# Kernel optimization log

Measured on AMD Instinct MI355X. Metric: run time of the kernel, lower is better.

Reference implementation:

```python
import jax, jax.numpy as jnp
import numpy as np

BS, R, W, N, H = 256, 4, 128, 2048, 256
TAU, ALPHA, EPS = 1.0, 0.7, 1e-8


def _l2norm(x, axis):
    return x / (jnp.linalg.norm(x, axis=axis, keepdims=True) + EPS)


def _gumbel(u):
    # standard Gumbel(0,1) from uniform samples
    return -jnp.log(-jnp.log(u + 1e-10) + 1e-10)


def setup_inputs() -> dict:
    key = jax.random.key(0)
    ks = jax.random.split(key, 10)
    return {
        "k_r": jax.random.normal(ks[0], (BS, R * W), jnp.float32),
        "m_t": jax.random.normal(ks[1], (BS, W), jnp.float32),
        "hx": jax.random.normal(ks[2], (1, BS, H), jnp.float32),
        "memory": jax.random.uniform(ks[3], (BS, W, N), jnp.float32),
        "usage": jax.random.uniform(ks[4], (BS, N), jnp.float32),
        "read_weights": jax.random.uniform(ks[5], (BS, R, N), jnp.float32),
        "Wg": jax.random.normal(ks[6], (H, 1), jnp.float32) / np.float32(np.sqrt(H)),
        "bg": jnp.zeros((1,), jnp.float32),
        "noise_write": jax.random.uniform(ks[7], (BS, 1, N), jnp.float32),
        "noise_read": jax.random.uniform(ks[8], (BS, R, N), jnp.float32),
        "m_idx": jax.random.randint(ks[9], (BS, N), 0, N).astype(jnp.int64),
        "seq_idx": N,
    }


def reference(k_r, m_t, hx, memory, usage, read_weights, Wg, bg,
              noise_write, noise_read, m_idx, seq_idx):
    # --- key / candidate preprocessing ---
    read_keys = jnp.tanh(k_r.reshape(BS, R, W))   # bs r W
    write_m = jnp.tanh(m_t.reshape(BS, 1, W))     # bs 1 W

    # --- usage bookkeeping (read weights detached as in torch) ---
    u_t = ALPHA * usage + (1.0 - ALPHA) * jax.lax.stop_gradient(read_weights).sum(axis=1)  # bs N

    # --- write (memory-full branch: content-addressed erase/update) ---
    # reversed cosine similarity between candidate and each slot
    dist = jnp.einsum('biw,bwn->bin', _l2norm(write_m, 2), _l2norm(memory, 1))  # bs 1 N
    gamma = jax.nn.sigmoid(hx[-1] @ Wg + bg)                                    # bs 1
    soft_wt = -dist + (gamma * u_t)[:, None, :]                                 # bs 1 N
    write_wt = jax.nn.softmax((1.0 - soft_wt + _gumbel(noise_write)) / TAU, axis=2)  # bs 1 N

    m_erased = jnp.einsum('bin,bwn->biw', write_wt, memory)                     # bs 1 W
    # M * (E - e^T w) + m^T w  with e = ones -> M*(1 - w) + m^T w
    mem_new = memory * (1.0 - write_wt) + jnp.einsum('biw,bin->bwn', write_m, write_wt)
    usage_new = u_t * (1.0 - jax.lax.stop_gradient(write_wt[:, 0, :]))          # bs N

    # --- read (gumbel-softmax content addressing on updated memory) ---
    dist_r = jnp.einsum('brw,bwn->brn', _l2norm(read_keys, 2), _l2norm(mem_new, 1))  # bs r N
    read_wt = jax.nn.softmax((dist_r + _gumbel(noise_read)) / TAU, axis=2)           # bs r N
    m_read = jnp.einsum('brn,bwn->brw', read_wt, mem_new)                            # bs r W

    return (m_read, mem_new, usage_new, read_wt, m_erased)
```

## Files before the change

### kernel.cpp

```cpp
#include <hip/hip_runtime.h>

#define BS   256
#define RR   4
#define WW   128
#define NN   2048
#define HH   256
#define NT   512
#define WH   64
#define NWAVE (NT / 64)
#define RPW  (WH / NWAVE)

typedef float nfloat4 __attribute__((ext_vector_type(4)));

__device__ __forceinline__ float wave_sum(float v) {
#pragma unroll
  for (int m = 32; m >= 1; m >>= 1) v += __shfl_xor(v, m, 64);
  return v;
}
__device__ __forceinline__ float wave_max(float v) {
#pragma unroll
  for (int m = 32; m >= 1; m >>= 1) v = fmaxf(v, __shfl_xor(v, m, 64));
  return v;
}
__device__ __forceinline__ float block_sum(float v, float* s_red) {
  const int tid = threadIdx.x;
  v = wave_sum(v);
  __syncthreads();
  if ((tid & 63) == 0) s_red[tid >> 6] = v;
  __syncthreads();
  float s = s_red[0];
#pragma unroll
  for (int i = 1; i < NWAVE; ++i) s += s_red[i];
  return s;
}
__device__ __forceinline__ float block_max(float v, float* s_red) {
  const int tid = threadIdx.x;
  v = wave_max(v);
  __syncthreads();
  if ((tid & 63) == 0) s_red[tid >> 6] = v;
  __syncthreads();
  float s = s_red[0];
#pragma unroll
  for (int i = 1; i < NWAVE; ++i) s = fmaxf(s, s_red[i]);
  return s;
}
__device__ __forceinline__ void block_max4(float v[RR], float* s_red4) {
  const int tid = threadIdx.x, lane = tid & 63, wid = tid >> 6;
#pragma unroll
  for (int m = 32; m >= 1; m >>= 1) {
#pragma unroll
    for (int r = 0; r < RR; ++r) v[r] = fmaxf(v[r], __shfl_xor(v[r], m, 64));
  }
  __syncthreads();
  if (lane == 0) {
#pragma unroll
    for (int r = 0; r < RR; ++r) s_red4[wid * RR + r] = v[r];
  }
  __syncthreads();
#pragma unroll
  for (int r = 0; r < RR; ++r) {
    float s = s_red4[r];
#pragma unroll
    for (int i = 1; i < NWAVE; ++i) s = fmaxf(s, s_red4[i * RR + r]);
    v[r] = s;
  }
}
__device__ __forceinline__ void block_sum4(float v[RR], float* s_red4) {
  const int tid = threadIdx.x, lane = tid & 63, wid = tid >> 6;
#pragma unroll
  for (int m = 32; m >= 1; m >>= 1) {
#pragma unroll
    for (int r = 0; r < RR; ++r) v[r] += __shfl_xor(v[r], m, 64);
  }
  __syncthreads();
  if (lane == 0) {
#pragma unroll
    for (int r = 0; r < RR; ++r) s_red4[wid * RR + r] = v[r];
  }
  __syncthreads();
#pragma unroll
  for (int r = 0; r < RR; ++r) {
    float s = s_red4[r];
#pragma unroll
    for (int i = 1; i < NWAVE; ++i) s += s_red4[i * RR + r];
    v[r] = s;
  }
}
__device__ __forceinline__ float gumbelf(float u) {
  return -logf(-logf(u + 1e-10f) + 1e-10f);
}

__global__ __launch_bounds__(NT) void k12_stats_softmax(
    const float* __restrict__ k_r, const float* __restrict__ m_t,
    const float* __restrict__ hx, const float* __restrict__ memory,
    const float* __restrict__ usage, const float* __restrict__ read_weights,
    const float* __restrict__ Wg, const float* __restrict__ bg,
    const float* __restrict__ noise_write, const float* __restrict__ noise_read,
    float* __restrict__ wt_out, float* __restrict__ usage_new,
    float* __restrict__ read_wt_out)
{
  __shared__ float s_wm[WW];
  __shared__ float s_rk[RR * WW];
  __shared__ float s_red[NWAVE * RR];
  __shared__ float s_rkinv[RR], s_rkwm[RR];

  const int b = blockIdx.x;
  const int tid = threadIdx.x;
  const int lane = tid & 63;
  const int wid = tid >> 6;
  const int c0 = 4 * tid;

  float gp = 0.f;
  if (tid < HH) gp = hx[(size_t)b * HH + tid] * Wg[tid];
  if (tid < WW) s_wm[tid] = tanhf(m_t[(size_t)b * WW + tid]);
  s_rk[tid] = tanhf(k_r[(size_t)b * (RR * WW) + tid]);

  float ut[4];
  {
    const size_t rb = (size_t)b * RR * NN;
    float4 u4 = *reinterpret_cast<const float4*>(usage + (size_t)b * NN + c0);
    float4 r0 = *reinterpret_cast<const float4*>(read_weights + rb + c0);
    float4 r1 = *reinterpret_cast<const float4*>(read_weights + rb + NN + c0);
    float4 r2 = *reinterpret_cast<const float4*>(read_weights + rb + 2 * NN + c0);
    float4 r3 = *reinterpret_cast<const float4*>(read_weights + rb + 3 * NN + c0);
    ut[0] = 0.7f * u4.x + 0.3f * (r0.x + r1.x + r2.x + r3.x);
    ut[1] = 0.7f * u4.y + 0.3f * (r0.y + r1.y + r2.y + r3.y);
    ut[2] = 0.7f * u4.z + 0.3f * (r0.z + r1.z + r2.z + r3.z);
    ut[3] = 0.7f * u4.w + 0.3f * (r0.w + r1.w + r2.w + r3.w);
  }

  const float gamma = 1.f / (1.f + expf(-(block_sum(gp, s_red) + bg[0])));
  float wmp = (tid < WW) ? s_wm[tid] * s_wm[tid] : 0.f;
  const float wmss = block_sum(wmp, s_red);
  const float inv_wm = 1.f / (sqrtf(wmss) + 1e-8f);

  if (wid < RR) {
    const float a = s_rk[wid * WW + lane];
    const float c = s_rk[wid * WW + 64 + lane];
    const float wa = s_wm[lane], wc = s_wm[64 + lane];
    float ss = wave_sum(a * a + c * c);
    float sw = wave_sum(a * wa + c * wc);
    if (lane == 0) {
      s_rkinv[wid] = 1.f / (sqrtf(ss) + 1e-8f);
      s_rkwm[wid] = sw;
    }
  }
  __syncthreads();

  const size_t base = (size_t)b * WW * NN;
  const float* Mb = memory + base;
  float cn[4] = {0.f, 0.f, 0.f, 0.f}, wd[4] = {0.f, 0.f, 0.f, 0.f};
  float rd[RR][4];
#pragma unroll
  for (int r = 0; r < RR; ++r) {
#pragma unroll
    for (int j = 0; j < 4; ++j) rd[r][j] = 0.f;
  }
#pragma unroll 8
  for (int w = 0; w < WW; ++w) {
    float4 v = *reinterpret_cast<const float4*>(Mb + (size_t)w * NN + c0);
    const float wmw = s_wm[w];
    cn[0] = fmaf(v.x, v.x, cn[0]); wd[0] = fmaf(wmw, v.x, wd[0]);
    cn[1] = fmaf(v.y, v.y, cn[1]); wd[1] = fmaf(wmw, v.y, wd[1]);
    cn[2] = fmaf(v.z, v.z, cn[2]); wd[2] = fmaf(wmw, v.z, wd[2]);
    cn[3] = fmaf(v.w, v.w, cn[3]); wd[3] = fmaf(wmw, v.w, wd[3]);
#pragma unroll
    for (int r = 0; r < RR; ++r) {
      const float rkw = s_rk[r * WW + w];
      rd[r][0] = fmaf(rkw, v.x, rd[r][0]);
      rd[r][1] = fmaf(rkw, v.y, rd[r][1]);
      rd[r][2] = fmaf(rkw, v.z, rd[r][2]);
      rd[r][3] = fmaf(rkw, v.w, rd[r][3]);
    }
  }

  float lg[4], mx = -1e30f;
  {
    float4 nw = *reinterpret_cast<const float4*>(noise_write + (size_t)b * NN + c0);
    const float nwv[4] = {nw.x, nw.y, nw.z, nw.w};
#pragma unroll
    for (int j = 0; j < 4; ++j) {
      float dist = wd[j] * inv_wm / (sqrtf(cn[j]) + 1e-8f);
      lg[j] = 1.f + dist - gamma * ut[j] + gumbelf(nwv[j]);
      mx = fmaxf(mx, lg[j]);
    }
  }
  mx = block_max(mx, s_red);
  float ex[4], es = 0.f;
#pragma unroll
  for (int j = 0; j < 4; ++j) { ex[j] = expf(lg[j] - mx); es += ex[j]; }
  es = block_sum(es, s_red);
  const float inv_es = 1.f / es;
  float wtk[4], omw[4];
#pragma unroll
  for (int j = 0; j < 4; ++j) { wtk[j] = ex[j] * inv_es; omw[j] = 1.f - wtk[j]; }
  {
    float4 un, wo;
    un.x = ut[0] * omw[0]; un.y = ut[1] * omw[1];
    un.z = ut[2] * omw[2]; un.w = ut[3] * omw[3];
    *reinterpret_cast<float4*>(usage_new + (size_t)b * NN + c0) = un;
    wo.x = wtk[0]; wo.y = wtk[1]; wo.z = wtk[2]; wo.w = wtk[3];
    *reinterpret_cast<float4*>(wt_out + (size_t)b * NN + c0) = wo;
  }

  const float invrk[RR] = { s_rkinv[0], s_rkinv[1], s_rkinv[2], s_rkinv[3] };
  const float rkwm[RR]  = { s_rkwm[0], s_rkwm[1], s_rkwm[2], s_rkwm[3] };
  float inv_cn2[4];
#pragma unroll
  for (int j = 0; j < 4; ++j) {
    float cn2 = omw[j] * omw[j] * cn[j]
              + 2.f * omw[j] * wtk[j] * wd[j]
              + wtk[j] * wtk[j] * wmss;
    inv_cn2[j] = 1.f / (sqrtf(cn2) + 1e-8f);
  }
  float lr[RR][4], mr[RR];
#pragma unroll
  for (int r = 0; r < RR; ++r) {
    float4 nr = *reinterpret_cast<const float4*>(
        noise_read + ((size_t)b * RR + r) * NN + c0);
    const float nrv[4] = {nr.x, nr.y, nr.z, nr.w};
    float m = -1e30f;
#pragma unroll
    for (int j = 0; j < 4; ++j) {
      float rdn = omw[j] * rd[r][j] + wtk[j] * rkwm[r];
      lr[r][j] = rdn * invrk[r] * inv_cn2[j] + gumbelf(nrv[j]);
      m = fmaxf(m, lr[r][j]);
    }
    mr[r] = m;
  }
  block_max4(mr, s_red);
  float er[RR][4], ers[RR];
#pragma unroll
  for (int r = 0; r < RR; ++r) {
    float s = 0.f;
#pragma unroll
    for (int j = 0; j < 4; ++j) { er[r][j] = expf(lr[r][j] - mr[r]); s += er[r][j]; }
    ers[r] = s;
  }
  block_sum4(ers, s_red);
#pragma unroll
  for (int r = 0; r < RR; ++r) {
    const float inv_ers = 1.f / ers[r];
    float4 o;
    o.x = er[r][0] * inv_ers; o.y = er[r][1] * inv_ers;
    o.z = er[r][2] * inv_ers; o.w = er[r][3] * inv_ers;
    *reinterpret_cast<float4*>(read_wt_out + ((size_t)b * RR + r) * NN + c0) = o;
  }
}

__global__ __launch_bounds__(NT, 2) void k3_apply(
    const float* __restrict__ m_t, const float* __restrict__ memory,
    const float* __restrict__ wt_in, const float* __restrict__ read_wt,
    float* __restrict__ mem_new, float* __restrict__ m_read,
    float* __restrict__ m_erased)
{
  __shared__ float s_wt[NN];
  __shared__ float s_rwt[RR][NN];

  const int bid = blockIdx.x;
  const int b = bid >> 1, rh = bid & 1;
  const int tid = threadIdx.x;
  const int lane = tid & 63;
  const int wid = tid >> 6;

  {
    const int c = 4 * tid;
    float4 w4 = *reinterpret_cast<const float4*>(wt_in + (size_t)b * NN + c);
    *reinterpret_cast<float4*>(&s_wt[c]) = w4;
#pragma unroll
    for (int r = 0; r < RR; ++r) {
      float4 t = *reinterpret_cast<const float4*>(
          read_wt + ((size_t)b * RR + r) * NN + c);
      *reinterpret_cast<float4*>(&s_rwt[r][c]) = t;
    }
  }
  const int w0 = wid * RPW;
  float wm[RPW];
#pragma unroll
  for (int i = 0; i < RPW; ++i)
    wm[i] = tanhf(m_t[(size_t)b * WW + rh * WH + w0 + i]);
  __syncthreads();

  const size_t hbase = (size_t)b * WW * NN + (size_t)rh * WH * NN;
  const float* Mb = memory + hbase;
  float* MNb = mem_new + hbase;

  float pme[RPW];
  float mrp[RPW][RR];
#pragma unroll
  for (int i = 0; i < RPW; ++i) {
    pme[i] = 0.f;
#pragma unroll
    for (int r = 0; r < RR; ++r) mrp[i][r] = 0.f;
  }

#pragma unroll 1
  for (int ch = 0; ch < NN; ch += 256) {
    const int c = ch + 4 * lane;
    const float4 wt4 = *reinterpret_cast<const float4*>(&s_wt[c]);
    const float ow0 = 1.f - wt4.x, ow1 = 1.f - wt4.y,
                ow2 = 1.f - wt4.z, ow3 = 1.f - wt4.w;
    float4 rw[RR];
#pragma unroll
    for (int r = 0; r < RR; ++r)
      rw[r] = *reinterpret_cast<const float4*>(&s_rwt[r][c]);

#pragma unroll
    for (int i = 0; i < RPW; ++i) {
      const size_t off = (size_t)(w0 + i) * NN + c;
      float4 v = *reinterpret_cast<const float4*>(Mb + off);
      float4 nv;
      nv.x = fmaf(v.x, ow0, wm[i] * wt4.x);
      nv.y = fmaf(v.y, ow1, wm[i] * wt4.y);
      nv.z = fmaf(v.z, ow2, wm[i] * wt4.z);
      nv.w = fmaf(v.w, ow3, wm[i] * wt4.w);
      nfloat4 nvv;
      nvv.x = nv.x; nvv.y = nv.y; nvv.z = nv.z; nvv.w = nv.w;
      __builtin_nontemporal_store(nvv, reinterpret_cast<nfloat4*>(MNb + off));
      float p = wt4.x * v.x;
      p = fmaf(wt4.y, v.y, p);
      p = fmaf(wt4.z, v.z, p);
      p = fmaf(wt4.w, v.w, p);
      pme[i] += p;
#pragma unroll
      for (int r = 0; r < RR; ++r) {
        float a = rw[r].x * nv.x;
        a = fmaf(rw[r].y, nv.y, a);
        a = fmaf(rw[r].z, nv.z, a);
        a = fmaf(rw[r].w, nv.w, a);
        mrp[i][r] += a;
      }
    }
  }

#pragma unroll
  for (int m = 32; m >= 1; m >>= 1) {
#pragma unroll
    for (int i = 0; i < RPW; ++i) {
      pme[i] += __shfl_xor(pme[i], m, 64);
#pragma unroll
      for (int r = 0; r < RR; ++r) mrp[i][r] += __shfl_xor(mrp[i][r], m, 64);
    }
  }
  if (lane == 0) {
    const int wg = rh * WH + w0;
#pragma unroll
    for (int i = 0; i < RPW; ++i) {
      m_erased[(size_t)b * WW + wg + i] = pme[i];
#pragma unroll
      for (int r = 0; r < RR; ++r)
        m_read[(size_t)b * RR * WW + r * WW + wg + i] = mrp[i][r];
    }
  }
}

extern "C" void kernel_launch(void* const* d_in, const int* in_sizes, int n_in,
                              void* d_out, int out_size, void* d_ws, size_t ws_size,
                              hipStream_t stream) {
  (void)in_sizes; (void)n_in; (void)ws_size; (void)out_size;
  const float* k_r          = (const float*)d_in[0];
  const float* m_t          = (const float*)d_in[1];
  const float* hx           = (const float*)d_in[2];
  const float* memory       = (const float*)d_in[3];
  const float* usage        = (const float*)d_in[4];
  const float* read_weights = (const float*)d_in[5];
  const float* Wg           = (const float*)d_in[6];
  const float* bg           = (const float*)d_in[7];
  const float* noise_write  = (const float*)d_in[8];
  const float* noise_read   = (const float*)d_in[9];

  float* out       = (float*)d_out;
  float* m_read    = out;
  float* mem_new   = m_read + (size_t)BS * RR * WW;
  float* usage_new = mem_new + (size_t)BS * WW * NN;
  float* read_wt   = usage_new + (size_t)BS * NN;
  float* m_erased  = read_wt + (size_t)BS * RR * NN;

  float* wt_ws = (float*)d_ws;

  k12_stats_softmax<<<dim3(BS), dim3(NT), 0, stream>>>(
      k_r, m_t, hx, memory, usage, read_weights, Wg, bg,
      noise_write, noise_read, wt_ws, usage_new, read_wt);
  k3_apply<<<dim3(2 * BS), dim3(NT), 0, stream>>>(
      m_t, memory, wt_ws, read_wt, mem_new, m_read, m_erased);
}
```

Baseline: 162.5 us.

## Split W reduction of stats kernel across two thread halves per block

The first kernel now launches 1024 threads per batch. Each half streams 64 of the 128 memory rows and accumulates partial norms and dot products, and the upper half hands its 24 partials to the lower half through padded shared memory. The aim is more memory-level parallelism and more waves in flight for the bandwidth-bound pass over memory, since only 256 blocks exist. The cost is about 51 KB of extra shared memory, which limits occupancy, plus an extra barrier, and the upper half sits idle through the softmax phases.

```diff
diff --git a/kernel.cpp b/kernel.cpp
--- a/kernel.cpp
+++ b/kernel.cpp
@@ -6,9 +6,13 @@
 #define NN   2048
 #define HH   256
 #define NT   512
+#define NT12 1024
 #define WH   64
-#define NWAVE (NT / 64)
+#define NWAVE 8
+#define NW12  16
 #define RPW  (WH / NWAVE)
+#define PCOMP 24
+#define PPAD  25
 
 typedef float nfloat4 __attribute__((ext_vector_type(4)));
 
@@ -22,6 +26,7 @@
   for (int m = 32; m >= 1; m >>= 1) v = fmaxf(v, __shfl_xor(v, m, 64));
   return v;
 }
+template<int NW>
 __device__ __forceinline__ float block_sum(float v, float* s_red) {
   const int tid = threadIdx.x;
   v = wave_sum(v);
@@ -30,9 +35,10 @@
   __syncthreads();
   float s = s_red[0];
 #pragma unroll
-  for (int i = 1; i < NWAVE; ++i) s += s_red[i];
+  for (int i = 1; i < NW; ++i) s += s_red[i];
   return s;
 }
+template<int NW>
 __device__ __forceinline__ float block_max(float v, float* s_red) {
   const int tid = threadIdx.x;
   v = wave_max(v);
@@ -41,9 +47,10 @@
   __syncthreads();
   float s = s_red[0];
 #pragma unroll
-  for (int i = 1; i < NWAVE; ++i) s = fmaxf(s, s_red[i]);
+  for (int i = 1; i < NW; ++i) s = fmaxf(s, s_red[i]);
   return s;
 }
+template<int NW>
 __device__ __forceinline__ void block_max4(float v[RR], float* s_red4) {
   const int tid = threadIdx.x, lane = tid & 63, wid = tid >> 6;
 #pragma unroll
@@ -61,10 +68,11 @@
   for (int r = 0; r < RR; ++r) {
     float s = s_red4[r];
 #pragma unroll
-    for (int i = 1; i < NWAVE; ++i) s = fmaxf(s, s_red4[i * RR + r]);
+    for (int i = 1; i < NW; ++i) s = fmaxf(s, s_red4[i * RR + r]);
     v[r] = s;
   }
 }
+template<int NW>
 __device__ __forceinline__ void block_sum4(float v[RR], float* s_red4) {
   const int tid = threadIdx.x, lane = tid & 63, wid = tid >> 6;
 #pragma unroll
@@ -82,7 +90,7 @@
   for (int r = 0; r < RR; ++r) {
     float s = s_red4[r];
 #pragma unroll
-    for (int i = 1; i < NWAVE; ++i) s += s_red4[i * RR + r];
+    for (int i = 1; i < NW; ++i) s += s_red4[i * RR + r];
     v[r] = s;
   }
 }
@@ -90,7 +98,7 @@
   return -logf(-logf(u + 1e-10f) + 1e-10f);
 }
 
-__global__ __launch_bounds__(NT) void k12_stats_softmax(
+__global__ __launch_bounds__(NT12, 4) void k12_stats_softmax(
     const float* __restrict__ k_r, const float* __restrict__ m_t,
     const float* __restrict__ hx, const float* __restrict__ memory,
     const float* __restrict__ usage, const float* __restrict__ read_weights,
@@ -101,22 +109,25 @@
 {
   __shared__ float s_wm[WW];
   __shared__ float s_rk[RR * WW];
-  __shared__ float s_red[NWAVE * RR];
+  __shared__ float s_part[512 * PPAD];
+  __shared__ float s_red[NW12 * RR];
   __shared__ float s_rkinv[RR], s_rkwm[RR];
 
   const int b = blockIdx.x;
   const int tid = threadIdx.x;
   const int lane = tid & 63;
   const int wid = tid >> 6;
-  const int c0 = 4 * tid;
+  const int half = tid >> 9;
+  const int t = tid & 511;
+  const int c0 = 4 * t;
 
   float gp = 0.f;
   if (tid < HH) gp = hx[(size_t)b * HH + tid] * Wg[tid];
   if (tid < WW) s_wm[tid] = tanhf(m_t[(size_t)b * WW + tid]);
-  s_rk[tid] = tanhf(k_r[(size_t)b * (RR * WW) + tid]);
-
-  float ut[4];
-  {
+  if (tid < RR * WW) s_rk[tid] = tanhf(k_r[(size_t)b * (RR * WW) + tid]);
+
+  float ut[4] = {0.f, 0.f, 0.f, 0.f};
+  if (half == 0) {
     const size_t rb = (size_t)b * RR * NN;
     float4 u4 = *reinterpret_cast<const float4*>(usage + (size_t)b * NN + c0);
     float4 r0 = *reinterpret_cast<const float4*>(read_weights + rb + c0);
@@ -129,9 +140,9 @@
     ut[3] = 0.7f * u4.w + 0.3f * (r0.w + r1.w + r2.w + r3.w);
   }
 
-  const float gamma = 1.f / (1.f + expf(-(block_sum(gp, s_red) + bg[0])));
+  const float gamma = 1.f / (1.f + expf(-(block_sum<NW12>(gp, s_red) + bg[0])));
   float wmp = (tid < WW) ? s_wm[tid] * s_wm[tid] : 0.f;
-  const float wmss = block_sum(wmp, s_red);
+  const float wmss = block_sum<NW12>(wmp, s_red);
   const float inv_wm = 1.f / (sqrtf(wmss) + 1e-8f);
 
   if (wid < RR) {
@@ -148,7 +159,7 @@
   __syncthreads();
 
   const size_t base = (size_t)b * WW * NN;
-  const float* Mb = memory + base;
+  const float* Mb = memory + base + (size_t)half * WH * NN;
   float cn[4] = {0.f, 0.f, 0.f, 0.f}, wd[4] = {0.f, 0.f, 0.f, 0.f};
   float rd[RR][4];
 #pragma unroll
@@ -156,17 +167,18 @@
 #pragma unroll
     for (int j = 0; j < 4; ++j) rd[r][j] = 0.f;
   }
+  const int rbase = half * WH;
 #pragma unroll 8
-  for (int w = 0; w < WW; ++w) {
+  for (int w = 0; w < WH; ++w) {
     float4 v = *reinterpret_cast<const float4*>(Mb + (size_t)w * NN + c0);
-    const float wmw = s_wm[w];
+    const float wmw = s_wm[rbase + w];
     cn[0] = fmaf(v.x, v.x, cn[0]); wd[0] = fmaf(wmw, v.x, wd[0]);
     cn[1] = fmaf(v.y, v.y, cn[1]); wd[1] = fmaf(wmw, v.y, wd[1]);
     cn[2] = fmaf(v.z, v.z, cn[2]); wd[2] = fmaf(wmw, v.z, wd[2]);
     cn[3] = fmaf(v.w, v.w, cn[3]); wd[3] = fmaf(wmw, v.w, wd[3]);
 #pragma unroll
     for (int r = 0; r < RR; ++r) {
-      const float rkw = s_rk[r * WW + w];
+      const float rkw = s_rk[r * WW + rbase + w];
       rd[r][0] = fmaf(rkw, v.x, rd[r][0]);
       rd[r][1] = fmaf(rkw, v.y, rd[r][1]);
       rd[r][2] = fmaf(rkw, v.z, rd[r][2]);
@@ -174,8 +186,30 @@
     }
   }
 
+  if (half == 1) {
+    float* p = &s_part[t * PPAD];
+#pragma unroll
+    for (int j = 0; j < 4; ++j) { p[j] = cn[j]; p[4 + j] = wd[j]; }
+#pragma unroll
+    for (int r = 0; r < RR; ++r) {
+#pragma unroll
+      for (int j = 0; j < 4; ++j) p[8 + r * 4 + j] = rd[r][j];
+    }
+  }
+  __syncthreads();
+  if (half == 0) {
+    const float* p = &s_part[t * PPAD];
+#pragma unroll
+    for (int j = 0; j < 4; ++j) { cn[j] += p[j]; wd[j] += p[4 + j]; }
+#pragma unroll
+    for (int r = 0; r < RR; ++r) {
+#pragma unroll
+      for (int j = 0; j < 4; ++j) rd[r][j] += p[8 + r * 4 + j];
+    }
+  }
+
   float lg[4], mx = -1e30f;
-  {
+  if (half == 0) {
     float4 nw = *reinterpret_cast<const float4*>(noise_write + (size_t)b * NN + c0);
     const float nwv[4] = {nw.x, nw.y, nw.z, nw.w};
 #pragma unroll
@@ -185,16 +219,18 @@
       mx = fmaxf(mx, lg[j]);
     }
   }
-  mx = block_max(mx, s_red);
-  float ex[4], es = 0.f;
-#pragma unroll
-  for (int j = 0; j < 4; ++j) { ex[j] = expf(lg[j] - mx); es += ex[j]; }
-  es = block_sum(es, s_red);
+  mx = block_max<NW12>(mx, s_red);
+  float ex[4] = {0.f, 0.f, 0.f, 0.f}, es = 0.f;
+  if (half == 0) {
+#pragma unroll
+    for (int j = 0; j < 4; ++j) { ex[j] = expf(lg[j] - mx); es += ex[j]; }
+  }
+  es = block_sum<NW12>(es, s_red);
   const float inv_es = 1.f / es;
   float wtk[4], omw[4];
 #pragma unroll
   for (int j = 0; j < 4; ++j) { wtk[j] = ex[j] * inv_es; omw[j] = 1.f - wtk[j]; }
-  {
+  if (half == 0) {
     float4 un, wo;
     un.x = ut[0] * omw[0]; un.y = ut[1] * omw[1];
     un.z = ut[2] * omw[2]; un.w = ut[3] * omw[3];
@@ -205,46 +241,57 @@
 
   const float invrk[RR] = { s_rkinv[0], s_rkinv[1], s_rkinv[2], s_rkinv[3] };
   const float rkwm[RR]  = { s_rkwm[0], s_rkwm[1], s_rkwm[2], s_rkwm[3] };
-  float inv_cn2[4];
-#pragma unroll
-  for (int j = 0; j < 4; ++j) {
-    float cn2 = omw[j] * omw[j] * cn[j]
-              + 2.f * omw[j] * wtk[j] * wd[j]
-              + wtk[j] * wtk[j] * wmss;
-    inv_cn2[j] = 1.f / (sqrtf(cn2) + 1e-8f);
-  }
   float lr[RR][4], mr[RR];
-#pragma unroll
-  for (int r = 0; r < RR; ++r) {
-    float4 nr = *reinterpret_cast<const float4*>(
-        noise_read + ((size_t)b * RR + r) * NN + c0);
-    const float nrv[4] = {nr.x, nr.y, nr.z, nr.w};
-    float m = -1e30f;
+  if (half == 0) {
+    float inv_cn2[4];
 #pragma unroll
     for (int j = 0; j < 4; ++j) {
-      float rdn = omw[j] * rd[r][j] + wtk[j] * rkwm[r];
-      lr[r][j] = rdn * invrk[r] * inv_cn2[j] + gumbelf(nrv[j]);
-      m = fmaxf(m, lr[r][j]);
-    }
-    mr[r] = m;
-  }
-  block_max4(mr, s_red);
+      float cn2 = omw[j] * omw[j] * cn[j]
+                + 2.f * omw[j] * wtk[j] * wd[j]
+                + wtk[j] * wtk[j] * wmss;
+      inv_cn2[j] = 1.f / (sqrtf(cn2) + 1e-8f);
+    }
+#pragma unroll
+    for (int r = 0; r < RR; ++r) {
+      float4 nr = *reinterpret_cast<const float4*>(
+          noise_read + ((size_t)b * RR + r) * NN + c0);
+      const float nrv[4] = {nr.x, nr.y, nr.z, nr.w};
+      float m = -1e30f;
+#pragma unroll
+      for (int j = 0; j < 4; ++j) {
+        float rdn = omw[j] * rd[r][j] + wtk[j] * rkwm[r];
+        lr[r][j] = rdn * invrk[r] * inv_cn2[j] + gumbelf(nrv[j]);
+        m = fmaxf(m, lr[r][j]);
+      }
+      mr[r] = m;
+    }
+  } else {
+#pragma unroll
+    for (int r = 0; r < RR; ++r) mr[r] = -1e30f;
+  }
+  block_max4<NW12>(mr, s_red);
   float er[RR][4], ers[RR];
 #pragma unroll
-  for (int r = 0; r < RR; ++r) {
-    float s = 0.f;
-#pragma unroll
-    for (int j = 0; j < 4; ++j) { er[r][j] = expf(lr[r][j] - mr[r]); s += er[r][j]; }
-    ers[r] = s;
-  }
-  block_sum4(ers, s_red);
-#pragma unroll
-  for (int r = 0; r < RR; ++r) {
-    const float inv_ers = 1.f / ers[r];
-    float4 o;
-    o.x = er[r][0] * inv_ers; o.y = er[r][1] * inv_ers;
-    o.z = er[r][2] * inv_ers; o.w = er[r][3] * inv_ers;
-    *reinterpret_cast<float4*>(read_wt_out + ((size_t)b * RR + r) * NN + c0) = o;
+  for (int r = 0; r < RR; ++r) ers[r] = 0.f;
+  if (half == 0) {
+#pragma unroll
+    for (int r = 0; r < RR; ++r) {
+      float s = 0.f;
+#pragma unroll
+      for (int j = 0; j < 4; ++j) { er[r][j] = expf(lr[r][j] - mr[r]); s += er[r][j]; }
+      ers[r] = s;
+    }
+  }
+  block_sum4<NW12>(ers, s_red);
+  if (half == 0) {
+#pragma unroll
+    for (int r = 0; r < RR; ++r) {
+      const float inv_ers = 1.f / ers[r];
+      float4 o;
+      o.x = er[r][0] * inv_ers; o.y = er[r][1] * inv_ers;
+      o.z = er[r][2] * inv_ers; o.w = er[r][3] * inv_ers;
+      *reinterpret_cast<float4*>(read_wt_out + ((size_t)b * RR + r) * NN + c0) = o;
+    }
   }
 }
 
@@ -378,7 +425,7 @@
 
   float* wt_ws = (float*)d_ws;
 
-  k12_stats_softmax<<<dim3(BS), dim3(NT), 0, stream>>>(
+  k12_stats_softmax<<<dim3(BS), dim3(NT12), 0, stream>>>(
       k_r, m_t, hx, memory, usage, read_weights, Wg, bg,
       noise_write, noise_read, wt_ws, usage_new, read_wt);
   k3_apply<<<dim3(2 * BS), dim3(NT), 0, stream>>>(
```

Result: slower. 166.7 us (+2.6%).

## Split memory stats pass into separate kernel with split-W reduction across thread halves

Applied to the files above, without the earlier changes.

The column-statistics pass over memory (norms, write dot, read dots) moves out of the fused softmax kernel into its own kernel. That kernel runs two blocks per batch, each covering half the columns, and splits the W dimension between two thread halves that are combined through shared memory. The goal is more parallelism and shorter serial loops over the memory read. In exchange it adds a kernel launch and writes the statistics to global memory, borrowing the mem_new output buffer as scratch, which the softmax kernel then reads back.

```diff
diff --git a/kernel.cpp b/kernel.cpp
--- a/kernel.cpp
+++ b/kernel.cpp
@@ -7,8 +7,10 @@
 #define HH   256
 #define NT   512
 #define WH   64
-#define NWAVE (NT / 64)
+#define NWAVE 8
+#define HCOL 1024
 #define RPW  (WH / NWAVE)
+#define PPAD 25
 
 typedef float nfloat4 __attribute__((ext_vector_type(4)));
 
@@ -90,12 +92,91 @@
   return -logf(-logf(u + 1e-10f) + 1e-10f);
 }
 
-__global__ __launch_bounds__(NT) void k12_stats_softmax(
+#define STAT(base, comp, b) ((base) + ((size_t)(comp) * BS + (b)) * NN)
+
+__global__ __launch_bounds__(NT, 4) void k1b_stats(
     const float* __restrict__ k_r, const float* __restrict__ m_t,
-    const float* __restrict__ hx, const float* __restrict__ memory,
-    const float* __restrict__ usage, const float* __restrict__ read_weights,
-    const float* __restrict__ Wg, const float* __restrict__ bg,
-    const float* __restrict__ noise_write, const float* __restrict__ noise_read,
+    const float* __restrict__ memory, float* __restrict__ stats)
+{
+  __shared__ float s_wm[WW];
+  __shared__ float s_rk[RR * WW];
+  __shared__ float s_part[256 * PPAD];
+
+  const int bid = blockIdx.x;
+  const int b = bid >> 1, h = bid & 1;
+  const int tid = threadIdx.x;
+  const int rh = tid >> 8;
+  const int tt = tid & 255;
+  const int cG = h * HCOL + 4 * tt;
+
+  if (tid < WW) s_wm[tid] = tanhf(m_t[(size_t)b * WW + tid]);
+  s_rk[tid] = tanhf(k_r[(size_t)b * (RR * WW) + tid]);
+  __syncthreads();
+
+  const float* Mb = memory + (size_t)b * WW * NN;
+  const int rbase = rh * WH;
+  float cn[4] = {0.f, 0.f, 0.f, 0.f}, wd[4] = {0.f, 0.f, 0.f, 0.f};
+  float rd[RR][4];
+#pragma unroll
+  for (int r = 0; r < RR; ++r) {
+#pragma unroll
+    for (int j = 0; j < 4; ++j) rd[r][j] = 0.f;
+  }
+#pragma unroll 8
+  for (int w = 0; w < WH; ++w) {
+    float4 v = *reinterpret_cast<const float4*>(Mb + (size_t)(rbase + w) * NN + cG);
+    const float wmw = s_wm[rbase + w];
+    cn[0] = fmaf(v.x, v.x, cn[0]); wd[0] = fmaf(wmw, v.x, wd[0]);
+    cn[1] = fmaf(v.y, v.y, cn[1]); wd[1] = fmaf(wmw, v.y, wd[1]);
+    cn[2] = fmaf(v.z, v.z, cn[2]); wd[2] = fmaf(wmw, v.z, wd[2]);
+    cn[3] = fmaf(v.w, v.w, cn[3]); wd[3] = fmaf(wmw, v.w, wd[3]);
+#pragma unroll
+    for (int r = 0; r < RR; ++r) {
+      const float rkw = s_rk[r * WW + rbase + w];
+      rd[r][0] = fmaf(rkw, v.x, rd[r][0]);
+      rd[r][1] = fmaf(rkw, v.y, rd[r][1]);
+      rd[r][2] = fmaf(rkw, v.z, rd[r][2]);
+      rd[r][3] = fmaf(rkw, v.w, rd[r][3]);
+    }
+  }
+
+  if (rh == 1) {
+    float* p = &s_part[tt * PPAD];
+#pragma unroll
+    for (int j = 0; j < 4; ++j) { p[j] = cn[j]; p[4 + j] = wd[j]; }
+#pragma unroll
+    for (int r = 0; r < RR; ++r) {
+#pragma unroll
+      for (int j = 0; j < 4; ++j) p[8 + r * 4 + j] = rd[r][j];
+    }
+  }
+  __syncthreads();
+  if (rh == 0) {
+    const float* p = &s_part[tt * PPAD];
+    float4 o;
+    o.x = cn[0] + p[0]; o.y = cn[1] + p[1];
+    o.z = cn[2] + p[2]; o.w = cn[3] + p[3];
+    *reinterpret_cast<float4*>(STAT(stats, 0, b) + cG) = o;
+    o.x = wd[0] + p[4]; o.y = wd[1] + p[5];
+    o.z = wd[2] + p[6]; o.w = wd[3] + p[7];
+    *reinterpret_cast<float4*>(STAT(stats, 1, b) + cG) = o;
+#pragma unroll
+    for (int r = 0; r < RR; ++r) {
+      o.x = rd[r][0] + p[8 + r * 4 + 0];
+      o.y = rd[r][1] + p[8 + r * 4 + 1];
+      o.z = rd[r][2] + p[8 + r * 4 + 2];
+      o.w = rd[r][3] + p[8 + r * 4 + 3];
+      *reinterpret_cast<float4*>(STAT(stats, 2 + r, b) + cG) = o;
+    }
+  }
+}
+
+__global__ __launch_bounds__(NT) void k2_softmax(
+    const float* __restrict__ k_r, const float* __restrict__ m_t,
+    const float* __restrict__ hx, const float* __restrict__ usage,
+    const float* __restrict__ read_weights, const float* __restrict__ Wg,
+    const float* __restrict__ bg, const float* __restrict__ noise_write,
+    const float* __restrict__ noise_read, const float* __restrict__ stats,
     float* __restrict__ wt_out, float* __restrict__ usage_new,
     float* __restrict__ read_wt_out)
 {
@@ -147,30 +228,16 @@
   }
   __syncthreads();
 
-  const size_t base = (size_t)b * WW * NN;
-  const float* Mb = memory + base;
-  float cn[4] = {0.f, 0.f, 0.f, 0.f}, wd[4] = {0.f, 0.f, 0.f, 0.f};
-  float rd[RR][4];
-#pragma unroll
-  for (int r = 0; r < RR; ++r) {
-#pragma unroll
-    for (int j = 0; j < 4; ++j) rd[r][j] = 0.f;
-  }
-#pragma unroll 8
-  for (int w = 0; w < WW; ++w) {
-    float4 v = *reinterpret_cast<const float4*>(Mb + (size_t)w * NN + c0);
-    const float wmw = s_wm[w];
-    cn[0] = fmaf(v.x, v.x, cn[0]); wd[0] = fmaf(wmw, v.x, wd[0]);
-    cn[1] = fmaf(v.y, v.y, cn[1]); wd[1] = fmaf(wmw, v.y, wd[1]);
-    cn[2] = fmaf(v.z, v.z, cn[2]); wd[2] = fmaf(wmw, v.z, wd[2]);
-    cn[3] = fmaf(v.w, v.w, cn[3]); wd[3] = fmaf(wmw, v.w, wd[3]);
+  float cn[4], wd[4], rdM[RR][4];
+  {
+    float4 a0 = *reinterpret_cast<const float4*>(STAT(stats, 0, b) + c0);
+    cn[0] = a0.x; cn[1] = a0.y; cn[2] = a0.z; cn[3] = a0.w;
+    float4 b0 = *reinterpret_cast<const float4*>(STAT(stats, 1, b) + c0);
+    wd[0] = b0.x; wd[1] = b0.y; wd[2] = b0.z; wd[3] = b0.w;
 #pragma unroll
     for (int r = 0; r < RR; ++r) {
-      const float rkw = s_rk[r * WW + w];
-      rd[r][0] = fmaf(rkw, v.x, rd[r][0]);
-      rd[r][1] = fmaf(rkw, v.y, rd[r][1]);
-      rd[r][2] = fmaf(rkw, v.z, rd[r][2]);
-      rd[r][3] = fmaf(rkw, v.w, rd[r][3]);
+      float4 d0 = *reinterpret_cast<const float4*>(STAT(stats, 2 + r, b) + c0);
+      rdM[r][0] = d0.x; rdM[r][1] = d0.y; rdM[r][2] = d0.z; rdM[r][3] = d0.w;
     }
   }
 
@@ -222,7 +289,7 @@
     float m = -1e30f;
 #pragma unroll
     for (int j = 0; j < 4; ++j) {
-      float rdn = omw[j] * rd[r][j] + wtk[j] * rkwm[r];
+      float rdn = omw[j] * rdM[r][j] + wtk[j] * rkwm[r];
       lr[r][j] = rdn * invrk[r] * inv_cn2[j] + gumbelf(nrv[j]);
       m = fmaxf(m, lr[r][j]);
     }
@@ -376,11 +443,13 @@
   float* read_wt   = usage_new + (size_t)BS * NN;
   float* m_erased  = read_wt + (size_t)BS * RR * NN;
 
+  float* stats = mem_new;
   float* wt_ws = (float*)d_ws;
 
-  k12_stats_softmax<<<dim3(BS), dim3(NT), 0, stream>>>(
-      k_r, m_t, hx, memory, usage, read_weights, Wg, bg,
-      noise_write, noise_read, wt_ws, usage_new, read_wt);
+  k1b_stats<<<dim3(2 * BS), dim3(NT), 0, stream>>>(k_r, m_t, memory, stats);
+  k2_softmax<<<dim3(BS), dim3(NT), 0, stream>>>(
+      k_r, m_t, hx, usage, read_weights, Wg, bg, noise_write, noise_read,
+      stats, wt_ws, usage_new, read_wt);
   k3_apply<<<dim3(2 * BS), dim3(NT), 0, stream>>>(
       m_t, memory, wt_ws, read_wt, mem_new, m_read, m_erased);
 }
```

After: 169.0 us. 4.0% more time.
